# Performance work log

Hardware: AMD Instinct MI355X
Metric: run time of the kernel (lower is better)

The kernel has to match this reference:

```python
import jax, jax.numpy as jnp
import numpy as np

KS = 3
ST = 1


def _windows(x, ks, st):
    """im2col sliding windows: (bs, c, h, w) -> (bs, c, H', W', ks, ks)
    where windows[b,c,i,j,k,f] = x[b,c, i*st+k, j*st+f] (matches torch as_strided)."""
    bs, c, h, w = x.shape
    Hp = (h - ks) // st + 1
    Wp = (w - ks) // st + 1
    return jnp.stack(
        [jnp.stack([x[:, :, k:k + Hp * st:st, f:f + Wp * st:st] for f in range(ks)], axis=-1)
         for k in range(ks)], axis=-2)


def setup_inputs() -> dict:
    key = jax.random.key(0)
    k1, k2, k3 = jax.random.split(key, 3)
    x = jax.random.normal(k1, (16, 16, 64, 512), dtype=jnp.float32)
    points = jax.random.normal(k2, (16, 3, 64, 512), dtype=jnp.float32)
    kernel = jax.random.normal(k3, (32, 16, 4), dtype=jnp.float32) * 0.05
    return {"x": x, "kernel": kernel, "points": points}


def reference(x, kernel, points):
    ks, st = KS, ST
    # (bs, in_c, H', W', ks, ks) overlapping patches of features and xyz coords
    strided_x = _windows(x, ks, st)
    strided_pts = _windows(points, ks, st)
    bd = ks // 2 if st == 1 else ks // 4
    # center point of each window: (bs, 3, H', W')
    ctr = points[:, :, bd:-bd, bd:-bd][:, :, ::st, ::st]
    # point-relative coordinates per window element: (bs, 3, H', W', ks, ks)
    rel_pts = ctr[..., None, None] - strided_pts
    # homogeneous coordinate -> d = 4
    rel_pts = jnp.concatenate([rel_pts, jnp.ones_like(rel_pts[:, :1])], axis=1)
    # kernel: (out_c, in_c, 4)
    return jnp.einsum('bdhwkf,bihwkf,oid->bohw', rel_pts, strided_x, kernel)
```

## Files before the change

kernel.cpp:

```cpp
#include <hip/hip_runtime.h>
#include <hip/hip_bf16.h>


#define HH 64
#define WW 512
#define HP 62
#define WP 510
#define IC 16
#define OC 32
#define BS 16
#define RB 2
#define TR (RB + 2)
#define TC 64

typedef __attribute__((ext_vector_type(8))) short short8;
typedef __attribute__((ext_vector_type(4))) float f32x4;

static __device__ __forceinline__ short f2bf(float f) {
    union { __hip_bfloat16 h; short s; } u;
    u.h = __float2bfloat16(f);
    return u.s;
}

__global__ __launch_bounds__(256) void flex_conv_direct(
    const float* __restrict__ x, const float* __restrict__ kern,
    const float* __restrict__ pts, float* __restrict__ out)
{
    const int tid = threadIdx.x;
    const int lane = tid & 63;
    const int wave = tid >> 6;
    const int p = lane & 15;
    const int c = lane >> 4;

    const int j0 = blockIdx.x * TC;
    const int i0 = blockIdx.y * RB;
    const int b = blockIdx.z;

    const int tc = wave * 16 + p;
    const int j = j0 + tc;
    int jc = j;
    if (jc > WW - 3) jc = WW - 3;

    const float* xb = x   + (size_t)b * IC * HH * WW + (size_t)i0 * WW + jc;
    const float* pb = pts + (size_t)b * 3  * HH * WW + (size_t)i0 * WW + jc;

    short8 a0lo, a0hi, a1lo, a1hi;
    {
        const float4* k0v = (const float4*)(kern + (size_t)p * 64 + c * 8);
        const float4* k1v = (const float4*)(kern + (size_t)(16 + p) * 64 + c * 8);
        float4 v0a = k0v[0], v0b = k0v[1], v0c = k0v[8], v0d = k0v[9];
        float4 v1a = k1v[0], v1b = k1v[1], v1c = k1v[8], v1d = k1v[9];
        a0lo[0]=f2bf(v0a.x); a0lo[1]=f2bf(v0a.y); a0lo[2]=f2bf(v0a.z); a0lo[3]=f2bf(v0a.w);
        a0lo[4]=f2bf(v0b.x); a0lo[5]=f2bf(v0b.y); a0lo[6]=f2bf(v0b.z); a0lo[7]=f2bf(v0b.w);
        a0hi[0]=f2bf(v0c.x); a0hi[1]=f2bf(v0c.y); a0hi[2]=f2bf(v0c.z); a0hi[3]=f2bf(v0c.w);
        a0hi[4]=f2bf(v0d.x); a0hi[5]=f2bf(v0d.y); a0hi[6]=f2bf(v0d.z); a0hi[7]=f2bf(v0d.w);
        a1lo[0]=f2bf(v1a.x); a1lo[1]=f2bf(v1a.y); a1lo[2]=f2bf(v1a.z); a1lo[3]=f2bf(v1a.w);
        a1lo[4]=f2bf(v1b.x); a1lo[5]=f2bf(v1b.y); a1lo[6]=f2bf(v1b.z); a1lo[7]=f2bf(v1b.w);
        a1hi[0]=f2bf(v1c.x); a1hi[1]=f2bf(v1c.y); a1hi[2]=f2bf(v1c.z); a1hi[3]=f2bf(v1c.w);
        a1hi[4]=f2bf(v1d.x); a1hi[5]=f2bf(v1d.y); a1hi[6]=f2bf(v1d.z); a1hi[7]=f2bf(v1d.w);
    }

    float xs[4][RB], px0[4][RB], px1[4][RB], px2[4][RB];
    #pragma unroll
    for (int t = 0; t < 4; ++t)
        #pragma unroll
        for (int q = 0; q < RB; ++q) { xs[t][q]=0.f; px0[t][q]=0.f; px1[t][q]=0.f; px2[t][q]=0.f; }
    float c0[RB], c1[RB], c2[RB];

    #pragma unroll
    for (int rr = 0; rr < TR; ++rr) {
        const float* q0 = pb + (size_t)rr * WW;
        const float* q1 = q0 + (size_t)HH * WW;
        const float* q2 = q1 + (size_t)HH * WW;
        const float pa0 = q0[0], pm0 = q0[1], pz0 = q0[2];
        const float pa1 = q1[0], pm1 = q1[1], pz1 = q1[2];
        const float pa2 = q2[0], pm2 = q2[1], pz2 = q2[2];
        if (rr >= 1 && rr <= RB) { c0[rr-1] = pm0; c1[rr-1] = pm1; c2[rr-1] = pm2; }
        #pragma unroll
        for (int t = 0; t < 4; ++t) {
            const int ic = (t >> 1) * 8 + 2 * c + (t & 1);
            const float* lx = xb + ((size_t)ic * HH + rr) * WW;
            const float x0 = lx[0], x1 = lx[1], x2 = lx[2];
            const float rsx = x0 + x1 + x2;
            float r0 = pa0 * x0; r0 = fmaf(pm0, x1, r0); r0 = fmaf(pz0, x2, r0);
            float r1 = pa1 * x0; r1 = fmaf(pm1, x1, r1); r1 = fmaf(pz1, x2, r1);
            float r2 = pa2 * x0; r2 = fmaf(pm2, x1, r2); r2 = fmaf(pz2, x2, r2);
            #pragma unroll
            for (int q = 0; q < RB; ++q) {
                if (rr >= q && rr <= q + 2) {
                    xs[t][q] += rsx; px0[t][q] += r0; px1[t][q] += r1; px2[t][q] += r2;
                }
            }
        }
    }

    #pragma unroll
    for (int q = 0; q < RB; ++q) {
        short8 blo, bhi;
        #pragma unroll
        for (int t = 0; t < 4; ++t) {
            const short t0 = f2bf(fmaf(c0[q], xs[t][q], -px0[t][q]));
            const short t1 = f2bf(fmaf(c1[q], xs[t][q], -px1[t][q]));
            const short t2 = f2bf(fmaf(c2[q], xs[t][q], -px2[t][q]));
            const short t3 = f2bf(xs[t][q]);
            const int s = (t & 1) * 4;
            if (t < 2) { blo[s+0]=t0; blo[s+1]=t1; blo[s+2]=t2; blo[s+3]=t3; }
            else       { bhi[s+0]=t0; bhi[s+1]=t1; bhi[s+2]=t2; bhi[s+3]=t3; }
        }
        f32x4 acc0 = {0.f,0.f,0.f,0.f}, acc1 = {0.f,0.f,0.f,0.f};
        acc0 = __builtin_amdgcn_mfma_f32_16x16x32_bf16(a0lo, blo, acc0, 0, 0, 0);
        acc0 = __builtin_amdgcn_mfma_f32_16x16x32_bf16(a0hi, bhi, acc0, 0, 0, 0);
        acc1 = __builtin_amdgcn_mfma_f32_16x16x32_bf16(a1lo, blo, acc1, 0, 0, 0);
        acc1 = __builtin_amdgcn_mfma_f32_16x16x32_bf16(a1hi, bhi, acc1, 0, 0, 0);
        if (j < WP) {
            float* ob = out + (size_t)b * OC * HP * WP + (size_t)(i0 + q) * WP + j;
            #pragma unroll
            for (int r = 0; r < 4; ++r) {
                const int o = c * 4 + r;
                ob[(size_t)o * HP * WP]        = acc0[r];
                ob[(size_t)(o + 16) * HP * WP] = acc1[r];
            }
        }
    }
}

extern "C" void kernel_launch(void* const* d_in, const int* in_sizes, int n_in,
                              void* d_out, int out_size, void* d_ws, size_t ws_size,
                              hipStream_t stream)
{
    const float* x    = (const float*)d_in[0];
    const float* kern = (const float*)d_in[1];
    const float* pts  = (const float*)d_in[2];
    float* out = (float*)d_out;

    dim3 block(256, 1, 1);
    dim3 grid(WW / TC, HP / RB, BS);
    flex_conv_direct<<<grid, block, 0, stream>>>(x, kern, pts, out);
}
```

Measured before the change: 123.4 us.

## Stream eight output rows per wave with a rolling three-row window

Each single-wave block now walks down eight output rows of a 16-column strip. It keeps per-row partial sums in a three-slot ring so every input row is loaded and reduced once, not once per overlapping window. This cuts redundant halo reads of x and points compared with two-row tiles. In exchange, blocks are smaller, the per-wave work is more serialized, and the tail tile is clamped, so some rows are recomputed.

After: 138.4 us. 12.2% more time.

```diff
diff --git a/kernel.cpp b/kernel.cpp
--- a/kernel.cpp
+++ b/kernel.cpp
@@ -9,9 +9,7 @@
 #define IC 16
 #define OC 32
 #define BS 16
-#define RB 2
-#define TR (RB + 2)
-#define TC 64
+#define NR 8
 
 typedef __attribute__((ext_vector_type(8))) short short8;
 typedef __attribute__((ext_vector_type(4))) float f32x4;
@@ -22,27 +20,26 @@
     return u.s;
 }
 
-__global__ __launch_bounds__(256) void flex_conv_direct(
+__global__ __launch_bounds__(64, 4) void flex_conv_col(
     const float* __restrict__ x, const float* __restrict__ kern,
     const float* __restrict__ pts, float* __restrict__ out)
 {
-    const int tid = threadIdx.x;
-    const int lane = tid & 63;
-    const int wave = tid >> 6;
+    const int lane = threadIdx.x;
     const int p = lane & 15;
     const int c = lane >> 4;
 
-    const int j0 = blockIdx.x * TC;
-    const int i0 = blockIdx.y * RB;
+    const int j0 = blockIdx.x * 16;
+    int i0 = blockIdx.y * NR;
+    if (i0 > HP - NR) i0 = HP - NR;
     const int b = blockIdx.z;
 
-    const int tc = wave * 16 + p;
-    const int j = j0 + tc;
+    const int j = j0 + p;
     int jc = j;
     if (jc > WW - 3) jc = WW - 3;
 
     const float* xb = x   + (size_t)b * IC * HH * WW + (size_t)i0 * WW + jc;
     const float* pb = pts + (size_t)b * 3  * HH * WW + (size_t)i0 * WW + jc;
+    float* const ob = out + (size_t)b * OC * HP * WP + j;
 
     short8 a0lo, a0hi, a1lo, a1hi;
     {
@@ -60,65 +57,61 @@
         a1hi[4]=f2bf(v1d.x); a1hi[5]=f2bf(v1d.y); a1hi[6]=f2bf(v1d.z); a1hi[7]=f2bf(v1d.w);
     }
 
-    float xs[4][RB], px0[4][RB], px1[4][RB], px2[4][RB];
-    #pragma unroll
-    for (int t = 0; t < 4; ++t)
-        #pragma unroll
-        for (int q = 0; q < RB; ++q) { xs[t][q]=0.f; px0[t][q]=0.f; px1[t][q]=0.f; px2[t][q]=0.f; }
-    float c0[RB], c1[RB], c2[RB];
+    float rsx[3][4], r0s[3][4], r1s[3][4], r2s[3][4];
+    float cm0[3], cm1[3], cm2[3];
 
     #pragma unroll
-    for (int rr = 0; rr < TR; ++rr) {
-        const float* q0 = pb + (size_t)rr * WW;
+    for (int ir = 0; ir < NR + 2; ++ir) {
+        const int sl = ir % 3;
+        const float* q0 = pb + (size_t)ir * WW;
         const float* q1 = q0 + (size_t)HH * WW;
         const float* q2 = q1 + (size_t)HH * WW;
         const float pa0 = q0[0], pm0 = q0[1], pz0 = q0[2];
         const float pa1 = q1[0], pm1 = q1[1], pz1 = q1[2];
         const float pa2 = q2[0], pm2 = q2[1], pz2 = q2[2];
-        if (rr >= 1 && rr <= RB) { c0[rr-1] = pm0; c1[rr-1] = pm1; c2[rr-1] = pm2; }
+        cm0[sl] = pm0; cm1[sl] = pm1; cm2[sl] = pm2;
         #pragma unroll
         for (int t = 0; t < 4; ++t) {
             const int ic = (t >> 1) * 8 + 2 * c + (t & 1);
-            const float* lx = xb + ((size_t)ic * HH + rr) * WW;
+            const float* lx = xb + ((size_t)ic * HH + ir) * WW;
             const float x0 = lx[0], x1 = lx[1], x2 = lx[2];
-            const float rsx = x0 + x1 + x2;
-            float r0 = pa0 * x0; r0 = fmaf(pm0, x1, r0); r0 = fmaf(pz0, x2, r0);
-            float r1 = pa1 * x0; r1 = fmaf(pm1, x1, r1); r1 = fmaf(pz1, x2, r1);
-            float r2 = pa2 * x0; r2 = fmaf(pm2, x1, r2); r2 = fmaf(pz2, x2, r2);
+            rsx[sl][t] = x0 + x1 + x2;
+            float a = pa0 * x0; a = fmaf(pm0, x1, a); a = fmaf(pz0, x2, a); r0s[sl][t] = a;
+            float d = pa1 * x0; d = fmaf(pm1, x1, d); d = fmaf(pz1, x2, d); r1s[sl][t] = d;
+            float e = pa2 * x0; e = fmaf(pm2, x1, e); e = fmaf(pz2, x2, e); r2s[sl][t] = e;
+        }
+        if (ir >= 2) {
+            const int io = i0 + ir - 2;
+            const int mid = (ir - 1) % 3;
+            const float cc0 = cm0[mid], cc1 = cm1[mid], cc2 = cm2[mid];
+            short8 blo, bhi;
             #pragma unroll
-            for (int q = 0; q < RB; ++q) {
-                if (rr >= q && rr <= q + 2) {
-                    xs[t][q] += rsx; px0[t][q] += r0; px1[t][q] += r1; px2[t][q] += r2;
+            for (int t = 0; t < 4; ++t) {
+                const float XS = rsx[0][t] + rsx[1][t] + rsx[2][t];
+                const float P0 = r0s[0][t] + r0s[1][t] + r0s[2][t];
+                const float P1 = r1s[0][t] + r1s[1][t] + r1s[2][t];
+                const float P2 = r2s[0][t] + r2s[1][t] + r2s[2][t];
+                const short t0 = f2bf(fmaf(cc0, XS, -P0));
+                const short t1 = f2bf(fmaf(cc1, XS, -P1));
+                const short t2 = f2bf(fmaf(cc2, XS, -P2));
+                const short t3 = f2bf(XS);
+                const int s = (t & 1) * 4;
+                if (t < 2) { blo[s+0]=t0; blo[s+1]=t1; blo[s+2]=t2; blo[s+3]=t3; }
+                else       { bhi[s+0]=t0; bhi[s+1]=t1; bhi[s+2]=t2; bhi[s+3]=t3; }
+            }
+            f32x4 acc0 = {0.f,0.f,0.f,0.f}, acc1 = {0.f,0.f,0.f,0.f};
+            acc0 = __builtin_amdgcn_mfma_f32_16x16x32_bf16(a0lo, blo, acc0, 0, 0, 0);
+            acc0 = __builtin_amdgcn_mfma_f32_16x16x32_bf16(a0hi, bhi, acc0, 0, 0, 0);
+            acc1 = __builtin_amdgcn_mfma_f32_16x16x32_bf16(a1lo, blo, acc1, 0, 0, 0);
+            acc1 = __builtin_amdgcn_mfma_f32_16x16x32_bf16(a1hi, bhi, acc1, 0, 0, 0);
+            if (j < WP) {
+                float* op = ob + (size_t)io * WP;
+                #pragma unroll
+                for (int r = 0; r < 4; ++r) {
+                    const int o = c * 4 + r;
+                    op[(size_t)o * HP * WP]        = acc0[r];
+                    op[(size_t)(o + 16) * HP * WP] = acc1[r];
                 }
-            }
-        }
-    }
-
-    #pragma unroll
-    for (int q = 0; q < RB; ++q) {
-        short8 blo, bhi;
-        #pragma unroll
-        for (int t = 0; t < 4; ++t) {
-            const short t0 = f2bf(fmaf(c0[q], xs[t][q], -px0[t][q]));
-            const short t1 = f2bf(fmaf(c1[q], xs[t][q], -px1[t][q]));
-            const short t2 = f2bf(fmaf(c2[q], xs[t][q], -px2[t][q]));
-            const short t3 = f2bf(xs[t][q]);
-            const int s = (t & 1) * 4;
-            if (t < 2) { blo[s+0]=t0; blo[s+1]=t1; blo[s+2]=t2; blo[s+3]=t3; }
-            else       { bhi[s+0]=t0; bhi[s+1]=t1; bhi[s+2]=t2; bhi[s+3]=t3; }
-        }
-        f32x4 acc0 = {0.f,0.f,0.f,0.f}, acc1 = {0.f,0.f,0.f,0.f};
-        acc0 = __builtin_amdgcn_mfma_f32_16x16x32_bf16(a0lo, blo, acc0, 0, 0, 0);
-        acc0 = __builtin_amdgcn_mfma_f32_16x16x32_bf16(a0hi, bhi, acc0, 0, 0, 0);
-        acc1 = __builtin_amdgcn_mfma_f32_16x16x32_bf16(a1lo, blo, acc1, 0, 0, 0);
-        acc1 = __builtin_amdgcn_mfma_f32_16x16x32_bf16(a1hi, bhi, acc1, 0, 0, 0);
-        if (j < WP) {
-            float* ob = out + (size_t)b * OC * HP * WP + (size_t)(i0 + q) * WP + j;
-            #pragma unroll
-            for (int r = 0; r < 4; ++r) {
-                const int o = c * 4 + r;
-                ob[(size_t)o * HP * WP]        = acc0[r];
-                ob[(size_t)(o + 16) * HP * WP] = acc1[r];
             }
         }
     }
@@ -133,7 +126,7 @@
     const float* pts  = (const float*)d_in[2];
     float* out = (float*)d_out;
 
-    dim3 block(256, 1, 1);
-    dim3 grid(WW / TC, HP / RB, BS);
-    flex_conv_direct<<<grid, block, 0, stream>>>(x, kern, pts, out);
+    dim3 block(64, 1, 1);
+    dim3 grid(WW / 16, (HP + NR - 1) / NR, BS);
+    flex_conv_col<<<grid, block, 0, stream>>>(x, kern, pts, out);
 }
```
